# Kernel tuning notes

Measured on AMD Instinct MI355X. Metric: run time of the kernel, lower is better.

Reference implementation:

```python
import jax, jax.numpy as jnp
import numpy as np

N = 100000      # num_nodes
E = 640000      # num_edges
D_IN = 128
D_OUT = 128
K = 3           # K_plus
ALPHA = 0.5
EXPONENT = -0.25


def setup_inputs() -> dict:
    key = jax.random.key(0)
    ks = jax.random.split(key, 7)
    return {
        "x_real": jax.random.normal(ks[0], (N, D_IN), dtype=jnp.float32),
        "x_imag": jax.random.normal(ks[1], (N, D_IN), dtype=jnp.float32),
        "W_real": jax.random.normal(ks[2], (K, D_OUT, D_IN), dtype=jnp.float32) * 0.05,
        "W_imag": jax.random.normal(ks[3], (K, D_OUT, D_IN), dtype=jnp.float32) * 0.05,
        "b_real": jax.random.normal(ks[4], (K, D_OUT), dtype=jnp.float32) * 0.05,
        "b_imag": jax.random.normal(ks[5], (K, D_OUT), dtype=jnp.float32) * 0.05,
        "edge_index": jax.random.randint(ks[6], (2, E), 0, N, dtype=jnp.int32),
    }


def _degnorm(deg, exponent):
    # deg^exponent with deg==0 -> 0 (inf masked), as in directed_norm
    return jnp.where(deg > 0, deg ** exponent, 0.0)


def reference(x_real, x_imag, W_real, W_imag, b_real, b_imag, edge_index):
    row, col = edge_index[0], edge_index[1]
    ones = jnp.ones(row.shape, dtype=x_real.dtype)
    deg_out = jax.ops.segment_sum(ones, row, num_segments=N)  # out-degree (adj row sums)
    deg_in = jax.ops.segment_sum(ones, col, num_segments=N)   # in-degree (adj col sums)
    # dir norm: D_out^exp @ A @ D_in^exp ; the transpose adj gets the same per-edge value
    val = _degnorm(deg_out, EXPONENT)[row] * _degnorm(deg_in, EXPONENT)[col]

    def spmm(dst, src, x):  # out[dst] += val * x[src]
        return jax.ops.segment_sum(val[:, None] * x[src], dst, num_segments=N)

    # Source recomputes identical adj@x every hop iteration -> compute once, reuse.
    y_r = spmm(row, col, x_real)
    y_i = spmm(row, col, x_imag)
    y_rt = spmm(col, row, x_real)
    y_it = spmm(col, row, x_imag)

    # exp weight penalty: hop i scaled by 1/2^i (i=0 scale 1)
    s = (0.5 ** jnp.arange(K)).astype(x_real.dtype)

    def combo(y, W, b):  # sum_i s_i * (y @ W[i]^T + b[i])
        return jnp.einsum('nd,kod,k->no', y, W, s) + s @ b

    sum_real_s2d = combo(y_r, W_real, b_real) - combo(y_i, W_imag, b_imag)
    sum_imag_s2d = combo(y_r, W_imag, b_imag) + combo(y_i, W_real, b_real)
    sum_real_d2s = combo(y_rt, W_real, b_real) - combo(y_it, W_imag, b_imag)
    # faithful to source: first term uses y_r (not y_rt)
    sum_imag_d2s = combo(y_r, W_imag, b_imag) + combo(y_it, W_real, b_real)

    total_real = ALPHA * sum_real_s2d + (1.0 - ALPHA) * sum_real_d2s
    total_imag = ALPHA * sum_imag_s2d + (1.0 - ALPHA) * sum_imag_d2s
    return total_real, total_imag
```

## Files before the change

kernel.cpp:

```cpp
#include <hip/hip_runtime.h>
#include <math.h>


typedef __bf16 bf16x8 __attribute__((ext_vector_type(8)));
typedef float f32x4 __attribute__((ext_vector_type(4)));

__device__ __forceinline__ unsigned short f2b(float f) {
    unsigned u = __float_as_uint(f);
    u += 0x7FFFu + ((u >> 16) & 1u);
    return (unsigned short)(u >> 16);
}
__device__ __forceinline__ unsigned pk(float lo, float hi) {
    return (unsigned)f2b(lo) | ((unsigned)f2b(hi) << 16);
}
__device__ __forceinline__ float2 b2f2(unsigned w) {
    return make_float2(__uint_as_float(w << 16), __uint_as_float(w & 0xFFFF0000u));
}

__global__ void count_kernel(const int* __restrict__ row, const int* __restrict__ col,
                             int* __restrict__ cnt, int N, int E) {
    int e = blockIdx.x * blockDim.x + threadIdx.x;
    if (e < E) {
        atomicAdd(&cnt[row[e]], 1);
        atomicAdd(&cnt[N + col[e]], 1);
    }
}

__global__ void scan1_kernel(const int* __restrict__ cnt, int* __restrict__ bsum,
                             float* __restrict__ dn, int n2) {
    __shared__ int tmp[256];
    int t = threadIdx.x, i = blockIdx.x * 256 + t;
    int d = (i < n2) ? cnt[i] : 0;
    if (i < n2) dn[i] = (d > 0) ? rsqrtf(sqrtf((float)d)) : 0.0f;
    tmp[t] = d;
    __syncthreads();
    for (int s = 128; s > 0; s >>= 1) {
        if (t < s) tmp[t] += tmp[t + s];
        __syncthreads();
    }
    if (t == 0) bsum[blockIdx.x] = tmp[0];
}

__global__ void scan2_kernel(int* __restrict__ bsum, int nb) {
    __shared__ int tmp[1024];
    int t = threadIdx.x;
    int v = (t < nb) ? bsum[t] : 0;
    tmp[t] = v;
    for (int d = 1; d < 1024; d <<= 1) {
        __syncthreads();
        int u = (t >= d) ? tmp[t - d] : 0;
        __syncthreads();
        tmp[t] += u;
    }
    __syncthreads();
    if (t < nb) bsum[t] = tmp[t] - v;
}

__global__ void scan3_kernel(const int* __restrict__ cnt, const int* __restrict__ bsum,
                             int* __restrict__ off, int n2) {
    __shared__ int tmp[256];
    int t = threadIdx.x, i = blockIdx.x * 256 + t;
    int v = (i < n2) ? cnt[i] : 0;
    tmp[t] = v;
    for (int d = 1; d < 256; d <<= 1) {
        __syncthreads();
        int u = (t >= d) ? tmp[t - d] : 0;
        __syncthreads();
        tmp[t] += u;
    }
    __syncthreads();
    if (i < n2) off[i] = tmp[t] - v + bsum[blockIdx.x];
}

__global__ void fill_kernel(const int* __restrict__ row, const int* __restrict__ col,
                            const float* __restrict__ dn,
                            int* __restrict__ off, int2* __restrict__ idx2, int N, int E) {
    int e = blockIdx.x * blockDim.x + threadIdx.x;
    if (e < E) {
        int r = row[e], c = col[e];
        int p = atomicAdd(&off[r], 1);
        idx2[p] = make_int2(c, __float_as_int(dn[N + c]));
        int q = atomicAdd(&off[N + c], 1);
        idx2[q] = make_int2(r, __float_as_int(dn[r]));
    }
}

__global__ void pack_kernel(const float4* __restrict__ xr4, const float4* __restrict__ xi4,
                            uint2* __restrict__ Xp2, int N) {
    int t = blockIdx.x * blockDim.x + threadIdx.x;
    if (t >= N * 32) return;
    int n = t >> 5, q = t & 31;
    float4 r = xr4[(size_t)n * 32 + q];
    float4 m = xi4[(size_t)n * 32 + q];
    Xp2[(size_t)n * 64 + q] = make_uint2(pk(r.x, r.y), pk(r.z, r.w));
    Xp2[(size_t)n * 64 + 32 + q] = make_uint2(pk(m.x, m.y), pk(m.z, m.w));
}

__global__ void weights_kernel(const float* __restrict__ Wr, const float* __restrict__ Wi,
                               const float* __restrict__ br, const float* __restrict__ bi,
                               unsigned short* __restrict__ Wt, float* __restrict__ bias) {
    int j = blockIdx.x * 256 + threadIdx.x;
    int k = j & 255, o = (j >> 8) & 127, path = j >> 15;
    int i = k & 127;
    float wr = Wr[o * 128 + i] + 0.5f * Wr[16384 + o * 128 + i] + 0.25f * Wr[32768 + o * 128 + i];
    float wi = Wi[o * 128 + i] + 0.5f * Wi[16384 + o * 128 + i] + 0.25f * Wi[32768 + o * 128 + i];
    float v;
    if (path == 0) v = (k < 128) ? wr : -wi;
    else           v = (k < 128) ? wr : wi;
    Wt[j] = f2b(v);
    if (j < 256) {
        int oo = j & 127, p = j >> 7;
        float er = br[oo] + 0.5f * br[128 + oo] + 0.25f * br[256 + oo];
        float ei = bi[oo] + 0.5f * bi[128 + oo] + 0.25f * bi[256 + oo];
        bias[j] = p ? (er + ei) : (er - ei);
    }
}

__global__ __launch_bounds__(256) void gather_kernel(
        const int* __restrict__ off, const int* __restrict__ cnt,
        const int2* __restrict__ idx2, const float* __restrict__ dn,
        const unsigned* __restrict__ Xp,
        unsigned int* __restrict__ A, int N) {
    int wave = (blockIdx.x * blockDim.x + threadIdx.x) >> 6;
    int lane = threadIdx.x & 63;
    if (wave >= N) return;
    int n = wave;

    float2 aR = {0.f, 0.f}, aI = {0.f, 0.f};
    {
        int end = off[n], start = end - cnt[n];
        for (int j = start; j < end; ++j) {
            int2 e = idx2[j];
            float w = __int_as_float(e.y);
            const unsigned* rp = Xp + (size_t)e.x * 128;
            float2 r = b2f2(rp[lane]);
            float2 m = b2f2(rp[64 + lane]);
            aR.x = fmaf(w, r.x, aR.x); aR.y = fmaf(w, r.y, aR.y);
            aI.x = fmaf(w, m.x, aI.x); aI.y = fmaf(w, m.y, aI.y);
        }
    }
    float2 bR = {0.f, 0.f}, bI = {0.f, 0.f};
    {
        int end = off[N + n], start = end - cnt[N + n];
        for (int j = start; j < end; ++j) {
            int2 e = idx2[j];
            float w = __int_as_float(e.y);
            const unsigned* rp = Xp + (size_t)e.x * 128;
            float2 r = b2f2(rp[lane]);
            float2 m = b2f2(rp[64 + lane]);
            bR.x = fmaf(w, r.x, bR.x); bR.y = fmaf(w, r.y, bR.y);
            bI.x = fmaf(w, m.x, bI.x); bI.y = fmaf(w, m.y, bI.y);
        }
    }
    float wo = dn[n], wi_ = dn[N + n];
    float yrx = wo * aR.x, yry = wo * aR.y;
    float ux = 0.5f * (yrx + wi_ * bR.x), uy = 0.5f * (yry + wi_ * bR.y);
    float vx = 0.5f * (wo * aI.x + wi_ * bI.x), vy = 0.5f * (wo * aI.y + wi_ * bI.y);
    unsigned int* rowp = A + (size_t)n * 192;
    rowp[lane]       = pk(ux, uy);
    rowp[64 + lane]  = pk(vx, vy);
    rowp[128 + lane] = pk(yrx, yry);
}

__global__ __launch_bounds__(256) void mfma_out_kernel(
        const unsigned short* __restrict__ A,
        const unsigned short* __restrict__ Wt,
        const float* __restrict__ bias,
        float* __restrict__ out, int N) {
    __shared__ unsigned short Alds[128 * 256];
    int path = blockIdx.y;
    int mbase = blockIdx.x * 128;
    int tid = threadIdx.x;
    int lane = tid & 63, wid = tid >> 6;

    const unsigned short* Ag = A + (size_t)mbase * 384 + path * 128;
#pragma unroll
    for (int i = 0; i < 16; ++i) {
        int linear = i * 256 + tid;
        int row = linear >> 5, chunk = linear & 31;
        int gchunk = chunk ^ (row & 7);
        const unsigned short* gp = Ag + (size_t)row * 384 + gchunk * 8;
        char* lp = (char*)Alds + (size_t)(i * 256 + wid * 64) * 16;
        __builtin_amdgcn_global_load_lds(
            (const __attribute__((address_space(1))) void*)gp,
            (__attribute__((address_space(3))) void*)lp, 16, 0, 0);
    }
    __syncthreads();

    int wm = wid >> 1, wn = wid & 1;
    int r0 = wm * 64, c0 = wn * 64;
    f32x4 acc[4][4] = {};
    const unsigned short* Wp = Wt + ((size_t)path * 128 + c0 + (lane & 15)) * 256 + (lane >> 4) * 8;

    for (int kk = 0; kk < 8; ++kk) {
        bf16x8 b[4];
#pragma unroll
        for (int ni = 0; ni < 4; ++ni)
            b[ni] = *(const bf16x8*)(Wp + (size_t)ni * 16 * 256 + kk * 32);
        bf16x8 a[4];
#pragma unroll
        for (int mi = 0; mi < 4; ++mi) {
            int row = r0 + mi * 16 + (lane & 15);
            int chunk = (kk * 4 + (lane >> 4)) ^ (row & 7);
            a[mi] = *(const bf16x8*)(Alds + row * 256 + chunk * 8);
        }
#pragma unroll
        for (int mi = 0; mi < 4; ++mi)
#pragma unroll
            for (int ni = 0; ni < 4; ++ni)
                acc[mi][ni] = __builtin_amdgcn_mfma_f32_16x16x32_bf16(a[mi], b[ni], acc[mi][ni], 0, 0, 0);
    }

    size_t ND = (size_t)N * 128;
#pragma unroll
    for (int mi = 0; mi < 4; ++mi) {
#pragma unroll
        for (int ni = 0; ni < 4; ++ni) {
            int col = c0 + ni * 16 + (lane & 15);
            float bb = bias[path * 128 + col];
#pragma unroll
            for (int r = 0; r < 4; ++r) {
                int n = mbase + r0 + mi * 16 + (lane >> 4) * 4 + r;
                if (n < N) out[(size_t)path * ND + (size_t)n * 128 + col] = acc[mi][ni][r] + bb;
            }
        }
    }
}

extern "C" void kernel_launch(void* const* d_in, const int* in_sizes, int n_in,
                              void* d_out, int out_size, void* d_ws, size_t ws_size,
                              hipStream_t stream) {
    const float* x_real = (const float*)d_in[0];
    const float* x_imag = (const float*)d_in[1];
    const float* W_real = (const float*)d_in[2];
    const float* W_imag = (const float*)d_in[3];
    const float* b_real = (const float*)d_in[4];
    const float* b_imag = (const float*)d_in[5];
    const int* edge = (const int*)d_in[6];

    int N = in_sizes[0] / 128;
    int E = in_sizes[6] / 2;
    const int* row = edge;
    const int* col = edge + E;
    float* out = (float*)d_out;

    char* ws = (char*)d_ws;
    int n2 = 2 * N;
    int Npad = ((N + 127) / 128) * 128;
    int* cnt = (int*)ws;
    int* off = (int*)(ws + (size_t)n2 * 4);
    int* bsum = (int*)(ws + (size_t)2 * n2 * 4);
    float* dn = (float*)(ws + (size_t)2 * n2 * 4 + 4096);
    int2* idx2 = (int2*)(ws + (size_t)3 * n2 * 4 + 4096);
    unsigned* Xp = (unsigned*)((char*)idx2 + (size_t)2 * E * 8);
    unsigned short* Wt = (unsigned short*)((char*)Xp + (size_t)N * 128 * 4);
    float* bias = (float*)((char*)Wt + 2 * 128 * 256 * 2);
    unsigned short* A = (unsigned short*)((char*)bias + 256 * 4);

    int nb = (n2 + 255) / 256;

    hipMemsetAsync(cnt, 0, (size_t)n2 * 4, stream);
    count_kernel<<<(E + 255) / 256, 256, 0, stream>>>(row, col, cnt, N, E);
    scan1_kernel<<<nb, 256, 0, stream>>>(cnt, bsum, dn, n2);
    scan2_kernel<<<1, 1024, 0, stream>>>(bsum, nb);
    scan3_kernel<<<nb, 256, 0, stream>>>(cnt, bsum, off, n2);
    fill_kernel<<<(E + 255) / 256, 256, 0, stream>>>(row, col, dn, off, idx2, N, E);
    pack_kernel<<<(N * 32 + 255) / 256, 256, 0, stream>>>((const float4*)x_real,
                                                          (const float4*)x_imag,
                                                          (uint2*)Xp, N);
    weights_kernel<<<256, 256, 0, stream>>>(W_real, W_imag, b_real, b_imag, Wt, bias);
    gather_kernel<<<(N * 64 + 255) / 256, 256, 0, stream>>>(off, cnt, idx2, dn,
                                                            Xp, (unsigned int*)A, N);
    dim3 gg(Npad / 128, 2);
    mfma_out_kernel<<<gg, 256, 0, stream>>>(A, Wt, bias, out, N);
}
```

Before: 539.1 us.

## Interleave packed real/imag features and unroll dual-list gather loop

The count kernel now records each edge's atomic rank, so the fill kernel writes CSR entries at off+rank without a second round of atomics. The packed feature layout interleaves real and imaginary bf16 pairs so each lane fetches one 8-byte load per neighbour instead of two 4-byte loads. The gather loop walks both adjacency lists together, unrolled by two, to keep four independent row loads in flight. This costs an extra rank buffer of 2E ints in workspace.

```diff
diff --git a/kernel.cpp b/kernel.cpp
--- a/kernel.cpp
+++ b/kernel.cpp
@@ -18,11 +18,11 @@
 }
 
 __global__ void count_kernel(const int* __restrict__ row, const int* __restrict__ col,
-                             int* __restrict__ cnt, int N, int E) {
+                             int* __restrict__ cnt, int* __restrict__ rank, int N, int E) {
     int e = blockIdx.x * blockDim.x + threadIdx.x;
     if (e < E) {
-        atomicAdd(&cnt[row[e]], 1);
-        atomicAdd(&cnt[N + col[e]], 1);
+        rank[e] = atomicAdd(&cnt[row[e]], 1);
+        rank[E + e] = atomicAdd(&cnt[N + col[e]], 1);
     }
 }
 
@@ -73,27 +73,26 @@
 }
 
 __global__ void fill_kernel(const int* __restrict__ row, const int* __restrict__ col,
-                            const float* __restrict__ dn,
-                            int* __restrict__ off, int2* __restrict__ idx2, int N, int E) {
+                            const float* __restrict__ dn, const int* __restrict__ off,
+                            const int* __restrict__ rank, int2* __restrict__ idx2,
+                            int N, int E) {
     int e = blockIdx.x * blockDim.x + threadIdx.x;
     if (e < E) {
         int r = row[e], c = col[e];
-        int p = atomicAdd(&off[r], 1);
-        idx2[p] = make_int2(c, __float_as_int(dn[N + c]));
-        int q = atomicAdd(&off[N + c], 1);
-        idx2[q] = make_int2(r, __float_as_int(dn[r]));
+        idx2[off[r] + rank[e]] = make_int2(c, __float_as_int(dn[N + c]));
+        idx2[off[N + c] + rank[E + e]] = make_int2(r, __float_as_int(dn[r]));
     }
 }
 
 __global__ void pack_kernel(const float4* __restrict__ xr4, const float4* __restrict__ xi4,
-                            uint2* __restrict__ Xp2, int N) {
+                            uint4* __restrict__ Xp4, int N) {
     int t = blockIdx.x * blockDim.x + threadIdx.x;
     if (t >= N * 32) return;
     int n = t >> 5, q = t & 31;
     float4 r = xr4[(size_t)n * 32 + q];
     float4 m = xi4[(size_t)n * 32 + q];
-    Xp2[(size_t)n * 64 + q] = make_uint2(pk(r.x, r.y), pk(r.z, r.w));
-    Xp2[(size_t)n * 64 + 32 + q] = make_uint2(pk(m.x, m.y), pk(m.z, m.w));
+    Xp4[(size_t)n * 32 + q] = make_uint4(pk(r.x, r.y), pk(m.x, m.y),
+                                         pk(r.z, r.w), pk(m.z, m.w));
 }
 
 __global__ void weights_kernel(const float* __restrict__ Wr, const float* __restrict__ Wi,
@@ -119,43 +118,85 @@
 __global__ __launch_bounds__(256) void gather_kernel(
         const int* __restrict__ off, const int* __restrict__ cnt,
         const int2* __restrict__ idx2, const float* __restrict__ dn,
-        const unsigned* __restrict__ Xp,
+        const uint2* __restrict__ Xp,
         unsigned int* __restrict__ A, int N) {
     int wave = (blockIdx.x * blockDim.x + threadIdx.x) >> 6;
     int lane = threadIdx.x & 63;
     if (wave >= N) return;
     int n = wave;
 
-    float2 aR = {0.f, 0.f}, aI = {0.f, 0.f};
-    {
-        int end = off[n], start = end - cnt[n];
-        for (int j = start; j < end; ++j) {
-            int2 e = idx2[j];
-            float w = __int_as_float(e.y);
-            const unsigned* rp = Xp + (size_t)e.x * 128;
-            float2 r = b2f2(rp[lane]);
-            float2 m = b2f2(rp[64 + lane]);
-            aR.x = fmaf(w, r.x, aR.x); aR.y = fmaf(w, r.y, aR.y);
-            aI.x = fmaf(w, m.x, aI.x); aI.y = fmaf(w, m.y, aI.y);
-        }
-    }
-    float2 bR = {0.f, 0.f}, bI = {0.f, 0.f};
-    {
-        int end = off[N + n], start = end - cnt[N + n];
-        for (int j = start; j < end; ++j) {
-            int2 e = idx2[j];
-            float w = __int_as_float(e.y);
-            const unsigned* rp = Xp + (size_t)e.x * 128;
-            float2 r = b2f2(rp[lane]);
-            float2 m = b2f2(rp[64 + lane]);
-            bR.x = fmaf(w, r.x, bR.x); bR.y = fmaf(w, r.y, bR.y);
-            bI.x = fmaf(w, m.x, bI.x); bI.y = fmaf(w, m.y, bI.y);
-        }
-    }
+    float aRx = 0.f, aRy = 0.f, aIx = 0.f, aIy = 0.f;
+    float bRx = 0.f, bRy = 0.f, bIx = 0.f, bIy = 0.f;
+    int s1 = off[n], c1 = cnt[n];
+    int s2 = off[N + n], c2 = cnt[N + n];
+    int k1 = 0, k2 = 0;
+    int L1 = c1 & ~1, L2 = c2 & ~1;
+
+    while (k1 < L1 && k2 < L2) {
+        int2 ea = idx2[s1 + k1], eb = idx2[s1 + k1 + 1];
+        int2 ec = idx2[s2 + k2], ed = idx2[s2 + k2 + 1];
+        uint2 da = Xp[(size_t)ea.x * 64 + lane];
+        uint2 db = Xp[(size_t)eb.x * 64 + lane];
+        uint2 dc = Xp[(size_t)ec.x * 64 + lane];
+        uint2 dd = Xp[(size_t)ed.x * 64 + lane];
+        float wa = __int_as_float(ea.y), wb = __int_as_float(eb.y);
+        float wc = __int_as_float(ec.y), wd = __int_as_float(ed.y);
+        float2 t;
+        t = b2f2(da.x); aRx = fmaf(wa, t.x, aRx); aRy = fmaf(wa, t.y, aRy);
+        t = b2f2(da.y); aIx = fmaf(wa, t.x, aIx); aIy = fmaf(wa, t.y, aIy);
+        t = b2f2(db.x); aRx = fmaf(wb, t.x, aRx); aRy = fmaf(wb, t.y, aRy);
+        t = b2f2(db.y); aIx = fmaf(wb, t.x, aIx); aIy = fmaf(wb, t.y, aIy);
+        t = b2f2(dc.x); bRx = fmaf(wc, t.x, bRx); bRy = fmaf(wc, t.y, bRy);
+        t = b2f2(dc.y); bIx = fmaf(wc, t.x, bIx); bIy = fmaf(wc, t.y, bIy);
+        t = b2f2(dd.x); bRx = fmaf(wd, t.x, bRx); bRy = fmaf(wd, t.y, bRy);
+        t = b2f2(dd.y); bIx = fmaf(wd, t.x, bIx); bIy = fmaf(wd, t.y, bIy);
+        k1 += 2; k2 += 2;
+    }
+    while (k1 < L1) {
+        int2 ea = idx2[s1 + k1], eb = idx2[s1 + k1 + 1];
+        uint2 da = Xp[(size_t)ea.x * 64 + lane];
+        uint2 db = Xp[(size_t)eb.x * 64 + lane];
+        float wa = __int_as_float(ea.y), wb = __int_as_float(eb.y);
+        float2 t;
+        t = b2f2(da.x); aRx = fmaf(wa, t.x, aRx); aRy = fmaf(wa, t.y, aRy);
+        t = b2f2(da.y); aIx = fmaf(wa, t.x, aIx); aIy = fmaf(wa, t.y, aIy);
+        t = b2f2(db.x); aRx = fmaf(wb, t.x, aRx); aRy = fmaf(wb, t.y, aRy);
+        t = b2f2(db.y); aIx = fmaf(wb, t.x, aIx); aIy = fmaf(wb, t.y, aIy);
+        k1 += 2;
+    }
+    while (k2 < L2) {
+        int2 ec = idx2[s2 + k2], ed = idx2[s2 + k2 + 1];
+        uint2 dc = Xp[(size_t)ec.x * 64 + lane];
+        uint2 dd = Xp[(size_t)ed.x * 64 + lane];
+        float wc = __int_as_float(ec.y), wd = __int_as_float(ed.y);
+        float2 t;
+        t = b2f2(dc.x); bRx = fmaf(wc, t.x, bRx); bRy = fmaf(wc, t.y, bRy);
+        t = b2f2(dc.y); bIx = fmaf(wc, t.x, bIx); bIy = fmaf(wc, t.y, bIy);
+        t = b2f2(dd.x); bRx = fmaf(wd, t.x, bRx); bRy = fmaf(wd, t.y, bRy);
+        t = b2f2(dd.y); bIx = fmaf(wd, t.x, bIx); bIy = fmaf(wd, t.y, bIy);
+        k2 += 2;
+    }
+    if (k1 < c1) {
+        int2 ea = idx2[s1 + k1];
+        uint2 da = Xp[(size_t)ea.x * 64 + lane];
+        float wa = __int_as_float(ea.y);
+        float2 t;
+        t = b2f2(da.x); aRx = fmaf(wa, t.x, aRx); aRy = fmaf(wa, t.y, aRy);
+        t = b2f2(da.y); aIx = fmaf(wa, t.x, aIx); aIy = fmaf(wa, t.y, aIy);
+    }
+    if (k2 < c2) {
+        int2 ec = idx2[s2 + k2];
+        uint2 dc = Xp[(size_t)ec.x * 64 + lane];
+        float wc = __int_as_float(ec.y);
+        float2 t;
+        t = b2f2(dc.x); bRx = fmaf(wc, t.x, bRx); bRy = fmaf(wc, t.y, bRy);
+        t = b2f2(dc.y); bIx = fmaf(wc, t.x, bIx); bIy = fmaf(wc, t.y, bIy);
+    }
+
     float wo = dn[n], wi_ = dn[N + n];
-    float yrx = wo * aR.x, yry = wo * aR.y;
-    float ux = 0.5f * (yrx + wi_ * bR.x), uy = 0.5f * (yry + wi_ * bR.y);
-    float vx = 0.5f * (wo * aI.x + wi_ * bI.x), vy = 0.5f * (wo * aI.y + wi_ * bI.y);
+    float yrx = wo * aRx, yry = wo * aRy;
+    float ux = 0.5f * (yrx + wi_ * bRx), uy = 0.5f * (yry + wi_ * bRy);
+    float vx = 0.5f * (wo * aIx + wi_ * bIx), vy = 0.5f * (wo * aIy + wi_ * bIy);
     unsigned int* rowp = A + (size_t)n * 192;
     rowp[lane]       = pk(ux, uy);
     rowp[64 + lane]  = pk(vx, vy);
@@ -251,23 +292,24 @@
     int* off = (int*)(ws + (size_t)n2 * 4);
     int* bsum = (int*)(ws + (size_t)2 * n2 * 4);
     float* dn = (float*)(ws + (size_t)2 * n2 * 4 + 4096);
-    int2* idx2 = (int2*)(ws + (size_t)3 * n2 * 4 + 4096);
-    unsigned* Xp = (unsigned*)((char*)idx2 + (size_t)2 * E * 8);
-    unsigned short* Wt = (unsigned short*)((char*)Xp + (size_t)N * 128 * 4);
+    int* rankp = (int*)(ws + (size_t)3 * n2 * 4 + 4096);
+    int2* idx2 = (int2*)((char*)rankp + (size_t)2 * E * 4);
+    uint2* Xp = (uint2*)((char*)idx2 + (size_t)2 * E * 8);
+    unsigned short* Wt = (unsigned short*)((char*)Xp + (size_t)N * 512);
     float* bias = (float*)((char*)Wt + 2 * 128 * 256 * 2);
     unsigned short* A = (unsigned short*)((char*)bias + 256 * 4);
 
     int nb = (n2 + 255) / 256;
 
     hipMemsetAsync(cnt, 0, (size_t)n2 * 4, stream);
-    count_kernel<<<(E + 255) / 256, 256, 0, stream>>>(row, col, cnt, N, E);
+    count_kernel<<<(E + 255) / 256, 256, 0, stream>>>(row, col, cnt, rankp, N, E);
     scan1_kernel<<<nb, 256, 0, stream>>>(cnt, bsum, dn, n2);
     scan2_kernel<<<1, 1024, 0, stream>>>(bsum, nb);
     scan3_kernel<<<nb, 256, 0, stream>>>(cnt, bsum, off, n2);
-    fill_kernel<<<(E + 255) / 256, 256, 0, stream>>>(row, col, dn, off, idx2, N, E);
+    fill_kernel<<<(E + 255) / 256, 256, 0, stream>>>(row, col, dn, off, rankp, idx2, N, E);
     pack_kernel<<<(N * 32 + 255) / 256, 256, 0, stream>>>((const float4*)x_real,
                                                           (const float4*)x_imag,
-                                                          (uint2*)Xp, N);
+                                                          (uint4*)Xp, N);
     weights_kernel<<<256, 256, 0, stream>>>(W_real, W_imag, b_real, b_imag, Wt, bias);
     gather_kernel<<<(N * 64 + 255) / 256, 256, 0, stream>>>(off, cnt, idx2, dn,
                                                             Xp, (unsigned int*)A, N);
```

Result: faster. 433.9 us (-19.5%).
